# Kernel tuning notes

Measured on AMD Instinct MI355X. Metric: run time of the kernel, lower is better.

Reference implementation:

```python
import jax, jax.numpy as jnp
import numpy as np

EPS = 1e-8
LAM = 1.0


def setup_inputs() -> dict:
    key = jax.random.key(0)
    k1, k2 = jax.random.split(key)
    B, H, W = 32, 512, 512
    output = jax.random.normal(k1, (B, 1, H, W), dtype=jnp.float32)
    target = jax.random.normal(k2, (B, 1, H, W), dtype=jnp.float32)
    return {"output": output, "target": target}


def _frc_loss(output, target):
    # squeeze channel dim: (B,1,H,W) -> (B,H,W)
    output = output[:, 0]
    target = target[:, 0]
    B, H, W = output.shape
    rnyquist = H // 2

    # radial index map (H,W): round(sqrt(fx^2 + fy^2)) in pixel-frequency units
    fx = jnp.fft.fftfreq(H, 1.0 / H)
    fy = jnp.fft.fftfreq(W, 1.0 / W)
    X, Y = jnp.meshgrid(fx, fy, indexing='ij')
    radial = jnp.round(jnp.sqrt(X ** 2 + Y ** 2)).astype(jnp.int32)
    # bins > rnyquist were ignored by the original loop -> dump into extra bin
    idx = jnp.where(radial > rnyquist, rnyquist + 1, radial).reshape(-1)  # (H*W,)

    F1 = jnp.fft.fft2(output, norm='forward')  # (B,H,W) complex
    F2 = jnp.fft.fft2(target, norm='forward')

    # per-pixel correlation terms, laid out (HW, B) for segment_sum over leading axis
    a = (F1.real * F2.real + F1.imag * F2.imag).reshape(B, -1).T
    b = (F1.imag * F2.real - F1.real * F2.imag).reshape(B, -1).T
    c1 = (F1.real ** 2 + F1.imag ** 2).reshape(B, -1).T
    c2 = (F2.real ** 2 + F2.imag ** 2).reshape(B, -1).T
    stacked = jnp.stack([a, b, c1, c2], axis=-1)  # (HW, B, 4)

    # single-pass radial-bin segment sum (replaces O(R*H*W) masked loop)
    sums = jax.ops.segment_sum(stacked, idx, num_segments=rnyquist + 2)
    sums = sums[:rnyquist + 1]  # drop overflow bin -> (rnyquist+1, B, 4)
    C_r, C_i, C1, C2 = sums[..., 0], sums[..., 1], sums[..., 2], sums[..., 3]

    frc = jnp.sqrt(C_r ** 2 + C_i ** 2) / (jnp.sqrt(C1 * C2) + EPS)
    return LAM * jnp.mean((1.0 - frc) ** 2)


def reference(output, target):
    return _frc_loss(output, target)
```

## Files before the change

### kernel.cpp

```cpp
#include <hip/hip_runtime.h>
#include <math.h>

#define NIMG  32
#define NRING 257
#define NB3   771
#define PI_F  3.14159265358979323846f

__device__ __forceinline__ float2 cadd(float2 a, float2 b){ return make_float2(a.x+b.x, a.y+b.y); }
__device__ __forceinline__ float2 csub(float2 a, float2 b){ return make_float2(a.x-b.x, a.y-b.y); }
__device__ __forceinline__ float2 cmul(float2 a, float2 b){ return make_float2(a.x*b.x - a.y*b.y, a.x*b.y + a.y*b.x); }
__device__ __forceinline__ float2 cmul_mi(float2 a){ return make_float2(a.y, -a.x); }

__device__ __forceinline__ float2 tw(const float2* T, int m){ return T[m + (m >> 3)]; }

__device__ __forceinline__ void dft8(float2* x) {
    const float c = 0.70710678118654752f;
    float2 u0 = cadd(x[0], x[4]), u1 = cadd(x[1], x[5]);
    float2 u2 = cadd(x[2], x[6]), u3 = cadd(x[3], x[7]);
    float2 v0 = csub(x[0], x[4]);
    float2 d1 = csub(x[1], x[5]);
    float2 v1 = make_float2(c*(d1.x + d1.y), c*(d1.y - d1.x));
    float2 d2 = csub(x[2], x[6]);
    float2 v2 = make_float2(d2.y, -d2.x);
    float2 d3 = csub(x[3], x[7]);
    float2 v3 = make_float2(-c*(d3.x - d3.y), -c*(d3.x + d3.y));
    float2 e0 = cadd(u0,u2), e1 = cadd(u1,u3);
    float2 f0 = csub(u0,u2), f1 = cmul_mi(csub(u1,u3));
    float2 g0 = cadd(v0,v2), g1 = cadd(v1,v3);
    float2 h0 = csub(v0,v2), h1 = cmul_mi(csub(v1,v3));
    x[0] = cadd(e0,e1); x[4] = csub(e0,e1);
    x[2] = cadd(f0,f1); x[6] = csub(f0,f1);
    x[1] = cadd(g0,g1); x[5] = csub(g0,g1);
    x[3] = cadd(h0,h1); x[7] = csub(h0,h1);
}

__device__ __forceinline__ void wave_fft512(float2* X, float2* Sw,
                                            const float2* T, int J) {
    dft8(X);
#pragma unroll
    for (int k = 1; k < 8; ++k) X[k] = cmul(X[k], tw(T, J * k));
    const int jj = J + (J >> 3);
#pragma unroll
    for (int k = 0; k < 8; ++k) Sw[jj + 72 * k] = X[k];
    __syncthreads();

    const int j2 = J & 7;
    const int bb = 72 * (J >> 3) + j2;
#pragma unroll
    for (int q = 0; q < 8; ++q) X[q] = Sw[bb + 9 * q];
    dft8(X);
#pragma unroll
    for (int k = 1; k < 8; ++k) X[k] = cmul(X[k], tw(T, 8 * j2 * k));
#pragma unroll
    for (int k = 0; k < 8; ++k) Sw[bb + 9 * k] = X[k];
    __syncthreads();

#pragma unroll
    for (int q = 0; q < 8; ++q) X[q] = Sw[9 * J + q];
    dft8(X);
}

__global__ __launch_bounds__(512) void fft_rows_T(const float* __restrict__ xr,
                                                  const float* __restrict__ yr,
                                                  float2* __restrict__ Zt) {
    __shared__ float2 S[8 * 576];
    __shared__ float2 T[576];
    const int t = threadIdx.x, w = t >> 6, J = t & 63;
    const int im = blockIdx.x >> 6, grp = blockIdx.x & 63;

    {
        float sw, cw;
        __sincosf(-2.0f * PI_F * (float)t / 512.0f, &sw, &cw);
        T[t + (t >> 3)] = make_float2(cw, sw);
    }

    const size_t rb = ((size_t)(im * 512 + grp * 8 + w)) << 9;
    float2 X[8];
#pragma unroll
    for (int q = 0; q < 8; ++q)
        X[q] = make_float2(xr[rb + J + 64 * q], yr[rb + J + 64 * q]);
    __syncthreads();

    wave_fft512(X, S + w * 576, T, J);
    __syncthreads();

    const int r = ((J & 7) << 3) | (J >> 3);
#pragma unroll
    for (int k = 0; k < 8; ++k) S[576 * k + 9 * r + w] = X[k];
    __syncthreads();

    float4* o4 = (float4*)(Zt + ((size_t)im << 18) + ((size_t)t << 9) + (grp << 3));
#pragma unroll
    for (int i = 0; i < 4; ++i) {
        float2 e0 = S[9 * t + 2 * i];
        float2 e1 = S[9 * t + 2 * i + 1];
        o4[i] = make_float4(e0.x, e0.y, e1.x, e1.y);
    }
}

__global__ __launch_bounds__(512) void fft_cols_rings(const float2* __restrict__ Zt,
                                                      float* __restrict__ sums) {
    __shared__ float2 S[8 * 576];
    __shared__ float2 T[576];
    __shared__ float  bins[258 * 3];
    const int t = threadIdx.x, w = t >> 6, J = t & 63;
    const int im = blockIdx.x >> 6, g = blockIdx.x & 63;

    {
        float sw, cw;
        __sincosf(-2.0f * PI_F * (float)t / 512.0f, &sw, &cw);
        T[t + (t >> 3)] = make_float2(cw, sw);
    }
    for (int i = t; i < 258 * 3; i += 512) bins[i] = 0.0f;

    int kxw;
    if (g == 0) kxw = (w < 4) ? w : ((w == 4) ? 256 : 504 + w);
    else        kxw = (w < 4) ? (4 * g + w) : (505 - 4 * g + w);

    const float2* rowp = Zt + ((size_t)im << 18) + ((size_t)kxw << 9);
    float2 X[8];
#pragma unroll
    for (int q = 0; q < 8; ++q) X[q] = rowp[J + 64 * q];
    __syncthreads();

    wave_fft512(X, S + w * 576, T, J);

    const int r = ((J & 7) << 3) | (J >> 3);
#pragma unroll
    for (int k = 0; k < 8; ++k) S[w * 576 + 64 * k + r] = X[k];
    __syncthreads();

    const int   ky  = t;
    const int   kyp = (512 - t) & 511;
    const float fxv = (ky < 256) ? (float)ky : (float)(ky - 512);
    const float fx2 = fxv * fxv;
    const float scale = 1.0f / (512.0f * 512.0f);

    auto pixel = [&](int u, int mu, float& av, float& c1, float& c2) {
        float2 zk = S[u  * 576 + ky];
        float2 zm = S[mu * 576 + kyp];
        float f1r = 0.5f * (zk.x + zm.x) * scale;
        float f1i = 0.5f * (zk.y - zm.y) * scale;
        float f2r = 0.5f * (zk.y + zm.y) * scale;
        float f2i = 0.5f * (zm.x - zk.x) * scale;
        av = f1r * f2r + f1i * f2i;
        c1 = f1r * f1r + f1i * f1i;
        c2 = f2r * f2r + f2i * f2i;
    };
    auto deposit = [&](float fy, float av, float c1, float c2) {
        int rr = (int)rintf(sqrtf(fx2 + fy * fy));
        if (rr > 256) rr = 257;
        atomicAdd(&bins[rr * 3 + 0], av);
        atomicAdd(&bins[rr * 3 + 1], c1);
        atomicAdd(&bins[rr * 3 + 2], c2);
    };

    if (g == 0) {
        float av, c1, c2;
        pixel(0, 0, av, c1, c2);  deposit(0.0f,   av, c1, c2);
        pixel(4, 4, av, c1, c2);  deposit(256.0f, av, c1, c2);
#pragma unroll
        for (int u = 1; u < 4; ++u) {
            float a1, b1, d1v, a2, b2, d2v;
            pixel(u,     8 - u, a1, b1, d1v);
            pixel(8 - u, u,     a2, b2, d2v);
            deposit((float)u, a1 + a2, b1 + b2, d1v + d2v);
        }
    } else {
#pragma unroll
        for (int u = 0; u < 4; ++u) {
            float a1, b1, d1v, a2, b2, d2v;
            pixel(u,     7 - u, a1, b1, d1v);
            pixel(7 - u, u,     a2, b2, d2v);
            deposit((float)(4 * g + u), a1 + a2, b1 + b2, d1v + d2v);
        }
    }
    __syncthreads();

    float* dstp = sums + (size_t)(im * 8 + (g & 7)) * NB3;
    for (int i = t; i < NB3; i += 512) atomicAdd(&dstp[i], bins[i]);
}

__global__ __launch_bounds__(256) void finalize(const float* __restrict__ sums,
                                                float* __restrict__ out) {
    const int b = blockIdx.x, t = threadIdx.x;
    float acc = 0.0f;
    for (int r = t; r < NRING; r += 256) {
        float cr = 0.f, c1 = 0.f, c2 = 0.f;
#pragma unroll
        for (int s = 0; s < 8; ++s) {
            const float* p = sums + (size_t)(b * 8 + s) * NB3 + r * 3;
            cr += p[0]; c1 += p[1]; c2 += p[2];
        }
        float frc = fabsf(cr) / (sqrtf(c1 * c2) + 1e-8f);
        float d = 1.0f - frc;
        acc += d * d;
    }
#pragma unroll
    for (int off = 32; off > 0; off >>= 1) acc += __shfl_down(acc, off);
    __shared__ float red[4];
    if ((t & 63) == 0) red[t >> 6] = acc;
    __syncthreads();
    if (t == 0)
        atomicAdd(out, (red[0] + red[1] + red[2] + red[3]) *
                       (1.0f / (NRING * (float)NIMG)));
}

extern "C" void kernel_launch(void* const* d_in, const int* in_sizes, int n_in,
                              void* d_out, int out_size, void* d_ws, size_t ws_size,
                              hipStream_t stream) {
    const float* xr = (const float*)d_in[0];
    const float* yr = (const float*)d_in[1];

    float2* Zt  = (float2*)d_ws;
    float*  sums = (float*)((char*)d_ws + (((size_t)NIMG << 18) * sizeof(float2)));

    hipMemsetAsync(sums, 0, (size_t)NIMG * 8 * NB3 * sizeof(float), stream);
    hipMemsetAsync(d_out, 0, sizeof(float), stream);

    fft_rows_T    <<<dim3(NIMG * 64), dim3(512), 0, stream>>>(xr, yr, Zt);
    fft_cols_rings<<<dim3(NIMG * 64), dim3(512), 0, stream>>>(Zt, sums);
    finalize      <<<dim3(NIMG), dim3(256), 0, stream>>>(sums, (float*)d_out);
}
```

Before: 216.8 us.

## Process two FFT rows per wave with 256-thread blocks and per-block partial sums

Both FFT kernels now use 256 threads, and each wave handles two 512-point transforms at once. This shares twiddle loads, gives more independent work per thread, and removes the intra-FFT __syncthreads, since each wave owns its own shared slices. The ring-binning step uses two interleaved shared bin copies with unsafeAtomicAdd to cut LDS atomic contention. When the workspace is large enough, each block writes its partials directly instead of using global atomics, which also removes the memset. Finalize then reduces 64 partials per image instead of 8.

```diff
diff --git a/kernel.cpp b/kernel.cpp
--- a/kernel.cpp
+++ b/kernel.cpp
@@ -1,16 +1,14 @@
 #include <hip/hip_runtime.h>
 #include <math.h>
 
-#define NIMG  32
-#define NRING 257
-#define NB3   771
-#define PI_F  3.14159265358979323846f
+#define NIMG 32
+#define NB3  771
+#define PI_F 3.14159265358979323846f
 
 __device__ __forceinline__ float2 cadd(float2 a, float2 b){ return make_float2(a.x+b.x, a.y+b.y); }
 __device__ __forceinline__ float2 csub(float2 a, float2 b){ return make_float2(a.x-b.x, a.y-b.y); }
 __device__ __forceinline__ float2 cmul(float2 a, float2 b){ return make_float2(a.x*b.x - a.y*b.y, a.x*b.y + a.y*b.x); }
 __device__ __forceinline__ float2 cmul_mi(float2 a){ return make_float2(a.y, -a.x); }
-
 __device__ __forceinline__ float2 tw(const float2* T, int m){ return T[m + (m >> 3)]; }
 
 __device__ __forceinline__ void dft8(float2* x) {
@@ -34,162 +32,196 @@
     x[3] = cadd(h0,h1); x[7] = csub(h0,h1);
 }
 
-__device__ __forceinline__ void wave_fft512(float2* X, float2* Sw,
-                                            const float2* T, int J) {
-    dft8(X);
-#pragma unroll
-    for (int k = 1; k < 8; ++k) X[k] = cmul(X[k], tw(T, J * k));
+__device__ __forceinline__ void wave_fft512_dual(float2* X0, float2* X1,
+                                                 float2* S0, float2* S1,
+                                                 const float2* T, int J) {
+    float2 W[8];
+    dft8(X0); dft8(X1);
+#pragma unroll
+    for (int k = 1; k < 8; ++k) W[k] = tw(T, J * k);
+#pragma unroll
+    for (int k = 1; k < 8; ++k) { X0[k] = cmul(X0[k], W[k]); X1[k] = cmul(X1[k], W[k]); }
     const int jj = J + (J >> 3);
 #pragma unroll
-    for (int k = 0; k < 8; ++k) Sw[jj + 72 * k] = X[k];
-    __syncthreads();
+    for (int k = 0; k < 8; ++k) { S0[jj + 72*k] = X0[k]; S1[jj + 72*k] = X1[k]; }
 
     const int j2 = J & 7;
     const int bb = 72 * (J >> 3) + j2;
 #pragma unroll
-    for (int q = 0; q < 8; ++q) X[q] = Sw[bb + 9 * q];
-    dft8(X);
-#pragma unroll
-    for (int k = 1; k < 8; ++k) X[k] = cmul(X[k], tw(T, 8 * j2 * k));
-#pragma unroll
-    for (int k = 0; k < 8; ++k) Sw[bb + 9 * k] = X[k];
-    __syncthreads();
-
-#pragma unroll
-    for (int q = 0; q < 8; ++q) X[q] = Sw[9 * J + q];
-    dft8(X);
-}
-
-__global__ __launch_bounds__(512) void fft_rows_T(const float* __restrict__ xr,
-                                                  const float* __restrict__ yr,
-                                                  float2* __restrict__ Zt) {
+    for (int q = 0; q < 8; ++q) { X0[q] = S0[bb + 9*q]; X1[q] = S1[bb + 9*q]; }
+    dft8(X0); dft8(X1);
+#pragma unroll
+    for (int k = 1; k < 8; ++k) W[k] = tw(T, 8 * j2 * k);
+#pragma unroll
+    for (int k = 1; k < 8; ++k) { X0[k] = cmul(X0[k], W[k]); X1[k] = cmul(X1[k], W[k]); }
+#pragma unroll
+    for (int k = 0; k < 8; ++k) { S0[bb + 9*k] = X0[k]; S1[bb + 9*k] = X1[k]; }
+
+#pragma unroll
+    for (int q = 0; q < 8; ++q) { X0[q] = S0[9*J + q]; X1[q] = S1[9*J + q]; }
+    dft8(X0); dft8(X1);
+}
+
+__global__ __launch_bounds__(256, 3) void fft_rows_T(const float* __restrict__ xr,
+                                                     const float* __restrict__ yr,
+                                                     float2* __restrict__ Zt) {
     __shared__ float2 S[8 * 576];
     __shared__ float2 T[576];
     const int t = threadIdx.x, w = t >> 6, J = t & 63;
     const int im = blockIdx.x >> 6, grp = blockIdx.x & 63;
 
-    {
+#pragma unroll
+    for (int i = 0; i < 2; ++i) {
+        const int m = t + 256 * i;
         float sw, cw;
-        __sincosf(-2.0f * PI_F * (float)t / 512.0f, &sw, &cw);
-        T[t + (t >> 3)] = make_float2(cw, sw);
-    }
-
-    const size_t rb = ((size_t)(im * 512 + grp * 8 + w)) << 9;
-    float2 X[8];
-#pragma unroll
-    for (int q = 0; q < 8; ++q)
-        X[q] = make_float2(xr[rb + J + 64 * q], yr[rb + J + 64 * q]);
-    __syncthreads();
-
-    wave_fft512(X, S + w * 576, T, J);
+        __sincosf(-2.0f * PI_F * (float)m / 512.0f, &sw, &cw);
+        T[m + (m >> 3)] = make_float2(cw, sw);
+    }
+
+    const size_t b0 = ((size_t)(im * 512 + grp * 8 + w)) << 9;
+    const size_t b1 = b0 + (4u << 9);
+    float2 X0[8], X1[8];
+#pragma unroll
+    for (int q = 0; q < 8; ++q) {
+        X0[q] = make_float2(xr[b0 + J + 64*q], yr[b0 + J + 64*q]);
+        X1[q] = make_float2(xr[b1 + J + 64*q], yr[b1 + J + 64*q]);
+    }
+    __syncthreads();
+
+    wave_fft512_dual(X0, X1, S + (2*w) * 576, S + (2*w + 1) * 576, T, J);
     __syncthreads();
 
     const int r = ((J & 7) << 3) | (J >> 3);
 #pragma unroll
-    for (int k = 0; k < 8; ++k) S[576 * k + 9 * r + w] = X[k];
-    __syncthreads();
-
-    float4* o4 = (float4*)(Zt + ((size_t)im << 18) + ((size_t)t << 9) + (grp << 3));
-#pragma unroll
-    for (int i = 0; i < 4; ++i) {
-        float2 e0 = S[9 * t + 2 * i];
-        float2 e1 = S[9 * t + 2 * i + 1];
-        o4[i] = make_float4(e0.x, e0.y, e1.x, e1.y);
-    }
-}
-
-__global__ __launch_bounds__(512) void fft_cols_rings(const float2* __restrict__ Zt,
-                                                      float* __restrict__ sums) {
+    for (int k = 0; k < 8; ++k) {
+        S[576*k + 9*r + w]     = X0[k];
+        S[576*k + 9*r + w + 4] = X1[k];
+    }
+    __syncthreads();
+
+#pragma unroll
+    for (int half = 0; half < 2; ++half) {
+        const int kx = t + 256 * half;
+        const int base = 576 * (kx >> 6) + 9 * (kx & 63);
+        float4* o4 = (float4*)(Zt + ((size_t)im << 18) + ((size_t)kx << 9) + (grp << 3));
+#pragma unroll
+        for (int i = 0; i < 4; ++i) {
+            float2 e0 = S[base + 2*i];
+            float2 e1 = S[base + 2*i + 1];
+            o4[i] = make_float4(e0.x, e0.y, e1.x, e1.y);
+        }
+    }
+}
+
+__global__ __launch_bounds__(256, 3) void fft_cols_rings(const float2* __restrict__ Zt,
+                                                         float* __restrict__ sums,
+                                                         int big) {
     __shared__ float2 S[8 * 576];
     __shared__ float2 T[576];
-    __shared__ float  bins[258 * 3];
+    __shared__ float  bins[2][774];
     const int t = threadIdx.x, w = t >> 6, J = t & 63;
     const int im = blockIdx.x >> 6, g = blockIdx.x & 63;
 
-    {
+#pragma unroll
+    for (int i = 0; i < 2; ++i) {
+        const int m = t + 256 * i;
         float sw, cw;
-        __sincosf(-2.0f * PI_F * (float)t / 512.0f, &sw, &cw);
-        T[t + (t >> 3)] = make_float2(cw, sw);
-    }
-    for (int i = t; i < 258 * 3; i += 512) bins[i] = 0.0f;
-
-    int kxw;
-    if (g == 0) kxw = (w < 4) ? w : ((w == 4) ? 256 : 504 + w);
-    else        kxw = (w < 4) ? (4 * g + w) : (505 - 4 * g + w);
-
-    const float2* rowp = Zt + ((size_t)im << 18) + ((size_t)kxw << 9);
-    float2 X[8];
-#pragma unroll
-    for (int q = 0; q < 8; ++q) X[q] = rowp[J + 64 * q];
-    __syncthreads();
-
-    wave_fft512(X, S + w * 576, T, J);
+        __sincosf(-2.0f * PI_F * (float)m / 512.0f, &sw, &cw);
+        T[m + (m >> 3)] = make_float2(cw, sw);
+    }
+    for (int i = t; i < 2 * 774; i += 256) bins[0][i] = 0.0f;
+
+    int c0, c1;
+    if (g == 0) { c0 = (w == 0) ? 0 : w; c1 = (w == 0) ? 256 : 512 - w; }
+    else        { c0 = 4 * g + w;        c1 = 512 - c0; }
+
+    const float2* rp0 = Zt + ((size_t)im << 18) + ((size_t)c0 << 9);
+    const float2* rp1 = Zt + ((size_t)im << 18) + ((size_t)c1 << 9);
+    float2 X0[8], X1[8];
+#pragma unroll
+    for (int q = 0; q < 8; ++q) { X0[q] = rp0[J + 64*q]; X1[q] = rp1[J + 64*q]; }
+    __syncthreads();
+
+    float2* S0 = S + (2*w) * 576;
+    float2* S1 = S + (2*w + 1) * 576;
+    wave_fft512_dual(X0, X1, S0, S1, T, J);
 
     const int r = ((J & 7) << 3) | (J >> 3);
 #pragma unroll
-    for (int k = 0; k < 8; ++k) S[w * 576 + 64 * k + r] = X[k];
-    __syncthreads();
-
-    const int   ky  = t;
-    const int   kyp = (512 - t) & 511;
-    const float fxv = (ky < 256) ? (float)ky : (float)(ky - 512);
-    const float fx2 = fxv * fxv;
+    for (int k = 0; k < 8; ++k) { S0[64*k + r] = X0[k]; S1[64*k + r] = X1[k]; }
+    __syncthreads();
+
     const float scale = 1.0f / (512.0f * 512.0f);
-
-    auto pixel = [&](int u, int mu, float& av, float& c1, float& c2) {
-        float2 zk = S[u  * 576 + ky];
-        float2 zm = S[mu * 576 + kyp];
+    float* bp = bins[t & 1];
+
+    auto pix = [&](float2 zk, float2 zm, float& av, float& c1v, float& c2v) {
         float f1r = 0.5f * (zk.x + zm.x) * scale;
         float f1i = 0.5f * (zk.y - zm.y) * scale;
         float f2r = 0.5f * (zk.y + zm.y) * scale;
         float f2i = 0.5f * (zm.x - zk.x) * scale;
-        av = f1r * f2r + f1i * f2i;
-        c1 = f1r * f1r + f1i * f1i;
-        c2 = f2r * f2r + f2i * f2i;
+        av  = f1r * f2r + f1i * f2i;
+        c1v = f1r * f1r + f1i * f1i;
+        c2v = f2r * f2r + f2i * f2i;
     };
-    auto deposit = [&](float fy, float av, float c1, float c2) {
-        int rr = (int)rintf(sqrtf(fx2 + fy * fy));
-        if (rr > 256) rr = 257;
-        atomicAdd(&bins[rr * 3 + 0], av);
-        atomicAdd(&bins[rr * 3 + 1], c1);
-        atomicAdd(&bins[rr * 3 + 2], c2);
-    };
-
-    if (g == 0) {
-        float av, c1, c2;
-        pixel(0, 0, av, c1, c2);  deposit(0.0f,   av, c1, c2);
-        pixel(4, 4, av, c1, c2);  deposit(256.0f, av, c1, c2);
-#pragma unroll
-        for (int u = 1; u < 4; ++u) {
-            float a1, b1, d1v, a2, b2, d2v;
-            pixel(u,     8 - u, a1, b1, d1v);
-            pixel(8 - u, u,     a2, b2, d2v);
-            deposit((float)u, a1 + a2, b1 + b2, d1v + d2v);
+
+#pragma unroll
+    for (int half = 0; half < 2; ++half) {
+        const int ky  = t + 256 * half;
+        const int kyp = (512 - ky) & 511;
+        const float fxv = (ky < 256) ? (float)ky : (float)(ky - 512);
+        const float fx2 = fxv * fxv;
+#pragma unroll
+        for (int u = 0; u < 4; ++u) {
+            const float2* A = S + (2*u) * 576;
+            const float2* B = S + (2*u + 1) * 576;
+            float2 zka = A[ky], zma = A[kyp];
+            float2 zkb = B[ky], zmb = B[kyp];
+            if (g == 0 && u == 0) {
+                float av, c1v, c2v;
+                pix(zka, zma, av, c1v, c2v);
+                int rr = (int)rintf(sqrtf(fx2));
+                if (rr > 256) rr = 257;
+                unsafeAtomicAdd(&bp[rr*3+0], av);
+                unsafeAtomicAdd(&bp[rr*3+1], c1v);
+                unsafeAtomicAdd(&bp[rr*3+2], c2v);
+                pix(zkb, zmb, av, c1v, c2v);
+                rr = (int)rintf(sqrtf(fx2 + 65536.0f));
+                if (rr > 256) rr = 257;
+                unsafeAtomicAdd(&bp[rr*3+0], av);
+                unsafeAtomicAdd(&bp[rr*3+1], c1v);
+                unsafeAtomicAdd(&bp[rr*3+2], c2v);
+            } else {
+                const float fy = (float)((g == 0) ? u : 4*g + u);
+                float a1, b1, d1, a2, b2, d2;
+                pix(zka, zmb, a1, b1, d1);
+                pix(zkb, zma, a2, b2, d2);
+                int rr = (int)rintf(sqrtf(fx2 + fy * fy));
+                if (rr > 256) rr = 257;
+                unsafeAtomicAdd(&bp[rr*3+0], a1 + a2);
+                unsafeAtomicAdd(&bp[rr*3+1], b1 + b2);
+                unsafeAtomicAdd(&bp[rr*3+2], d1 + d2);
+            }
         }
+    }
+    __syncthreads();
+
+    if (big) {
+        float* dst = sums + (size_t)blockIdx.x * NB3;
+        for (int i = t; i < NB3; i += 256) dst[i] = bins[0][i] + bins[1][i];
     } else {
-#pragma unroll
-        for (int u = 0; u < 4; ++u) {
-            float a1, b1, d1v, a2, b2, d2v;
-            pixel(u,     7 - u, a1, b1, d1v);
-            pixel(7 - u, u,     a2, b2, d2v);
-            deposit((float)(4 * g + u), a1 + a2, b1 + b2, d1v + d2v);
-        }
-    }
-    __syncthreads();
-
-    float* dstp = sums + (size_t)(im * 8 + (g & 7)) * NB3;
-    for (int i = t; i < NB3; i += 512) atomicAdd(&dstp[i], bins[i]);
+        float* dst = sums + (size_t)(im * 8 + (g & 7)) * NB3;
+        for (int i = t; i < NB3; i += 256) unsafeAtomicAdd(&dst[i], bins[0][i] + bins[1][i]);
+    }
 }
 
 __global__ __launch_bounds__(256) void finalize(const float* __restrict__ sums,
-                                                float* __restrict__ out) {
+                                                float* __restrict__ out, int spi) {
     const int b = blockIdx.x, t = threadIdx.x;
     float acc = 0.0f;
-    for (int r = t; r < NRING; r += 256) {
+    for (int r = t; r < 257; r += 256) {
         float cr = 0.f, c1 = 0.f, c2 = 0.f;
-#pragma unroll
-        for (int s = 0; s < 8; ++s) {
-            const float* p = sums + (size_t)(b * 8 + s) * NB3 + r * 3;
+        for (int s = 0; s < spi; ++s) {
+            const float* p = sums + (size_t)(b * spi + s) * NB3 + r * 3;
             cr += p[0]; c1 += p[1]; c2 += p[2];
         }
         float frc = fabsf(cr) / (sqrtf(c1 * c2) + 1e-8f);
@@ -202,8 +234,8 @@
     if ((t & 63) == 0) red[t >> 6] = acc;
     __syncthreads();
     if (t == 0)
-        atomicAdd(out, (red[0] + red[1] + red[2] + red[3]) *
-                       (1.0f / (NRING * (float)NIMG)));
+        unsafeAtomicAdd(out, (red[0] + red[1] + red[2] + red[3]) *
+                             (1.0f / (257.0f * (float)NIMG)));
 }
 
 extern "C" void kernel_launch(void* const* d_in, const int* in_sizes, int n_in,
@@ -212,13 +244,16 @@
     const float* xr = (const float*)d_in[0];
     const float* yr = (const float*)d_in[1];
 
-    float2* Zt  = (float2*)d_ws;
-    float*  sums = (float*)((char*)d_ws + (((size_t)NIMG << 18) * sizeof(float2)));
-
-    hipMemsetAsync(sums, 0, (size_t)NIMG * 8 * NB3 * sizeof(float), stream);
+    float2* Zt = (float2*)d_ws;
+    const size_t ztBytes = ((size_t)NIMG << 18) * sizeof(float2);
+    float* sums = (float*)((char*)d_ws + ztBytes);
+    const int big = (ws_size >= ztBytes + (size_t)2048 * NB3 * sizeof(float)) ? 1 : 0;
+
+    if (!big)
+        hipMemsetAsync(sums, 0, (size_t)NIMG * 8 * NB3 * sizeof(float), stream);
     hipMemsetAsync(d_out, 0, sizeof(float), stream);
 
-    fft_rows_T    <<<dim3(NIMG * 64), dim3(512), 0, stream>>>(xr, yr, Zt);
-    fft_cols_rings<<<dim3(NIMG * 64), dim3(512), 0, stream>>>(Zt, sums);
-    finalize      <<<dim3(NIMG), dim3(256), 0, stream>>>(sums, (float*)d_out);
-}
+    fft_rows_T    <<<dim3(NIMG * 64), dim3(256), 0, stream>>>(xr, yr, Zt);
+    fft_cols_rings<<<dim3(NIMG * 64), dim3(256), 0, stream>>>(Zt, sums, big);
+    finalize      <<<dim3(NIMG), dim3(256), 0, stream>>>(sums, (float*)d_out, big ? 64 : 8);
+}
```

Result: slower. 231.3 us (+6.7%).
